# Performance work log

Measured on AMD Instinct MI355X. Metric: run time of the kernel, lower is better.

## Reference

```python
import jax, jax.numpy as jnp
import numpy as np

N_HEAD = 16

def setup_inputs() -> dict:
    key = jax.random.key(0)
    ks = jax.random.split(key, 5)
    B, T, D = 2, 2048, 1024
    k = D // N_HEAD
    scale = 0.02
    return {
        'x': jax.random.normal(ks[0], (B, T, D), dtype=jnp.float32),
        'Wq': jax.random.normal(ks[1], (D, D), dtype=jnp.float32) * scale,
        'Wk': jax.random.normal(ks[2], (D, k), dtype=jnp.float32) * scale,
        'Wv': jax.random.normal(ks[3], (D, k), dtype=jnp.float32) * scale,
        'Wo': jax.random.normal(ks[4], (D, D), dtype=jnp.float32) * scale,
    }

def reference(x, Wq, Wk, Wv, Wo):
    B, T, D = x.shape
    h = N_HEAD
    k = D // h
    Q = (x @ Wq).reshape(B, T, h, k)          # per-head queries
    K = x @ Wk                                 # single shared K head: (B,T,k)
    V = x @ Wv                                 # single shared V head: (B,T,k)
    scores = jnp.einsum('bthk,bsk->bhts', Q, K) / jnp.sqrt(jnp.float32(k))
    causal = jnp.tril(jnp.ones((T, T), dtype=bool))  # (T,T)
    scores = jnp.where(causal[None, None, :, :], scores, -jnp.inf)
    A = jax.nn.softmax(scores, axis=-1)        # (B,h,T,T)
    Y = jnp.einsum('bhts,bsk->bthk', A, V).reshape(B, T, D)
    return Y @ Wo
```

## Files before the change

kernel.cpp:

```cpp
#include <hip/hip_runtime.h>
#include <hip/hip_bf16.h>
#include <stdint.h>

typedef short short8 __attribute__((ext_vector_type(8)));
typedef float f32x4 __attribute__((ext_vector_type(4)));

constexpr int SEQ   = 2048;
constexpr int DM    = 1024;
constexpr int NHEAD = 16;
constexpr int HD    = 64;
constexpr int LDQ   = 1152;
constexpr int BATCH = 2;

__device__ __forceinline__ unsigned short f2bf(float f) {
    union { float f; uint32_t u; } v; v.f = f;
    uint32_t u = v.u;
    uint32_t r = (u + 0x7fffu + ((u >> 16) & 1u)) >> 16;
    return (unsigned short)r;
}

typedef __attribute__((address_space(1))) const void gvoid_t;
typedef __attribute__((address_space(3))) void lvoid_t;
__device__ __forceinline__ void gload16(const void* g, void* l) {
    __builtin_amdgcn_global_load_lds((gvoid_t*)g, (lvoid_t*)l, 16, 0, 0);
}

__global__ __launch_bounds__(256) void cast_x_kernel(
        const float* __restrict__ x, unsigned short* __restrict__ xb, int n) {
    int i = (blockIdx.x * 256 + threadIdx.x) * 4;
    if (i >= n) return;
    const float4 v = *(const float4*)(x + i);
    ushort4 o;
    o.x = f2bf(v.x); o.y = f2bf(v.y); o.z = f2bf(v.z); o.w = f2bf(v.w);
    *(ushort4*)(xb + i) = o;
}

__global__ __launch_bounds__(256) void prep_w_kernel(
        const float* __restrict__ Wq, const float* __restrict__ Wk,
        const float* __restrict__ Wv, const float* __restrict__ Wo,
        unsigned short* __restrict__ wtq, unsigned short* __restrict__ wot) {
    __shared__ unsigned short tile[32][33];
    int z = blockIdx.z;
    const float* W; unsigned short* Wt; int C;
    if (z == 0)      { W = Wq; Wt = wtq;                              C = DM; }
    else if (z == 1) { W = Wk; Wt = wtq + (size_t)DM * DM;            C = HD; }
    else if (z == 2) { W = Wv; Wt = wtq + (size_t)(DM + HD) * DM;     C = HD; }
    else             { W = Wo; Wt = wot;                              C = DM; }
    int c0 = blockIdx.x * 32, r0 = blockIdx.y * 32;
    if (c0 >= C) return;
    int tx = threadIdx.x & 31, ty = threadIdx.x >> 5;
    for (int i = ty; i < 32; i += 8)
        tile[i][tx] = f2bf(W[(size_t)(r0 + i) * C + (c0 + tx)]);
    __syncthreads();
    for (int i = ty; i < 32; i += 8)
        Wt[(size_t)(c0 + i) * DM + (r0 + tx)] = tile[tx][i];
}

__global__ __launch_bounds__(256) void gemm_bt_kernel(
        const unsigned short* __restrict__ A,
        const unsigned short* __restrict__ Bt,
        void* __restrict__ Cout,
        unsigned short* __restrict__ VtOut,
        int M, int N, int K, int out_bf16) {
    __shared__ unsigned short ldsA[2][2][128 * 32];
    __shared__ unsigned short ldsB[2][2][64 * 32];
    int lane = threadIdx.x & 63, wave = threadIdx.x >> 6;
    int ln = lane & 15, quad = lane >> 4;
    int wm = wave >> 1, wn = wave & 1;
    int m0 = blockIdx.y * 128, n0 = blockIdx.x * 64;

    int srow = lane >> 2, scol = (lane & 3) * 8;
    const unsigned short* gA0 = A + (size_t)(m0 + wave * 32 + srow) * K + scol;
    const unsigned short* gA1 = gA0 + (size_t)16 * K;
    const unsigned short* gB0 = Bt + (size_t)(n0 + wave * 16 + srow) * K + scol;

    f32x4 acc[4][2];
    for (int i = 0; i < 4; ++i)
        for (int jj = 0; jj < 2; ++jj) acc[i][jj] = f32x4{0, 0, 0, 0};

    auto stage = [&](int k0, int buf) {
#pragma unroll
        for (int hh = 0; hh < 2; ++hh) {
            gload16(gA0 + k0 + hh * 32, &ldsA[buf][hh][wave * 1024]);
            gload16(gA1 + k0 + hh * 32, &ldsA[buf][hh][wave * 1024 + 512]);
            gload16(gB0 + k0 + hh * 32, &ldsB[buf][hh][wave * 512]);
        }
    };

    stage(0, 0);
    int niter = K >> 6;
    for (int it = 0; it < niter; ++it) {
        __syncthreads();
        if (it + 1 < niter) stage((it + 1) << 6, (it + 1) & 1);
        int buf = it & 1;
        short8 aF[2][4], bF[2][2];
#pragma unroll
        for (int hh = 0; hh < 2; ++hh) {
#pragma unroll
            for (int i = 0; i < 4; ++i)
                aF[hh][i] = *(const short8*)&ldsA[buf][hh][(wm * 64 + i * 16 + ln) * 32 + quad * 8];
#pragma unroll
            for (int jj = 0; jj < 2; ++jj)
                bF[hh][jj] = *(const short8*)&ldsB[buf][hh][(wn * 32 + jj * 16 + ln) * 32 + quad * 8];
        }
#pragma unroll
        for (int hh = 0; hh < 2; ++hh)
#pragma unroll
            for (int mt = 0; mt < 4; ++mt)
#pragma unroll
                for (int nt = 0; nt < 2; ++nt)
                    acc[mt][nt] = __builtin_amdgcn_mfma_f32_16x16x32_bf16(
                        aF[hh][mt], bF[hh][nt], acc[mt][nt], 0, 0, 0);
    }

    if (out_bf16) {
        unsigned short* C = (unsigned short*)Cout;
#pragma unroll
        for (int mt = 0; mt < 4; ++mt)
            for (int nt = 0; nt < 2; ++nt)
                for (int r = 0; r < 4; ++r) {
                    int row = m0 + wm * 64 + mt * 16 + quad * 4 + r;
                    int col = n0 + wn * 32 + nt * 16 + ln;
                    C[(size_t)row * N + col] = f2bf(acc[mt][nt][r]);
                }
        if (VtOut != nullptr && n0 == DM + HD) {
#pragma unroll
            for (int mt = 0; mt < 4; ++mt)
                for (int nt = 0; nt < 2; ++nt)
                    for (int r = 0; r < 4; ++r) {
                        int row = m0 + wm * 64 + mt * 16 + quad * 4 + r;
                        int d = wn * 32 + nt * 16 + ln;
                        int bb = row >> 11, s = row & 2047;
                        VtOut[((size_t)bb * HD + d) * SEQ + s] = f2bf(acc[mt][nt][r]);
                    }
        }
    } else {
        float* C = (float*)Cout;
#pragma unroll
        for (int mt = 0; mt < 4; ++mt)
            for (int nt = 0; nt < 2; ++nt)
                for (int r = 0; r < 4; ++r) {
                    int row = m0 + wm * 64 + mt * 16 + quad * 4 + r;
                    int col = n0 + wn * 32 + nt * 16 + ln;
                    C[(size_t)row * N + col] = acc[mt][nt][r];
                }
    }
}

__global__ __launch_bounds__(256) void attn_kernel(
        const unsigned short* __restrict__ QKV,
        const unsigned short* __restrict__ Vt,
        unsigned short* __restrict__ Y) {
    __shared__ unsigned short ldsK[2][64 * 64];
    __shared__ unsigned short ldsV[2][64 * 64];
    __shared__ unsigned short pbuf[4][16][72];

    int lane = threadIdx.x & 63, wave = threadIdx.x >> 6;
    int ln = lane & 15, quad = lane >> 4;
    int bid = blockIdx.x;
    int jg = 31 - (bid >> 5);
    int bh = bid & 31;
    int h = bh & 15, b = bh >> 4;
    int q0 = (jg * 4 + wave) * 16;
    const size_t baseRow = (size_t)b * SEQ;
    const unsigned short* Vb = Vt + (size_t)b * HD * SEQ;

    int t = threadIdx.x;
    int trow = t >> 3, tcb = t & 7;
    int cbg = tcb ^ (trow & 7);
    const unsigned short* gK = QKV + (baseRow + trow) * LDQ + DM + cbg * 8;
    const unsigned short* gV = Vb + (size_t)trow * SEQ + cbg * 8;
    int dstoff = trow * 64 + tcb * 8;

    auto stageKV = [&](int s0n, int buf) {
#pragma unroll
        for (int rr = 0; rr < 2; ++rr) {
            gload16(gK + (size_t)(s0n + 32 * rr) * LDQ, &ldsK[buf][dstoff + rr * 2048]);
            gload16(gV + (size_t)32 * rr * SEQ + s0n,   &ldsV[buf][dstoff + rr * 2048]);
        }
    };

    short8 aQ0, aQ1;
    {
        const unsigned short* qp = QKV + (baseRow + q0 + ln) * LDQ + h * HD + quad * 8;
        aQ0 = *(const short8*)(qp);
        aQ1 = *(const short8*)(qp + 32);
    }

    float lsum[4] = {0.f, 0.f, 0.f, 0.f};
    f32x4 o[4];
    for (int nt = 0; nt < 4; ++nt) o[nt] = f32x4{0, 0, 0, 0};

    const float c_exp = 0.1803368802f;

    auto computeStep = [&](int s0, int buf, bool partial) {
        const unsigned short* Kb = ldsK[buf];
        const unsigned short* Vf = ldsV[buf];
#pragma unroll
        for (int c = 0; c < 4; ++c) {
            int kbase = s0 + c * 16;
            if (partial && kbase > q0 + 15) {
#pragma unroll
                for (int r = 0; r < 4; ++r)
                    pbuf[wave][quad * 4 + r][c * 16 + ln] = 0;
                continue;
            }
            short8 k0f = *(const short8*)&Kb[(c * 16 + ln) * 64 + ((quad ^ (ln & 7)) * 8)];
            short8 k1f = *(const short8*)&Kb[(c * 16 + ln) * 64 + (((4 + quad) ^ (ln & 7)) * 8)];
            f32x4 s = {0, 0, 0, 0};
            s = __builtin_amdgcn_mfma_f32_16x16x32_bf16(aQ0, k0f, s, 0, 0, 0);
            s = __builtin_amdgcn_mfma_f32_16x16x32_bf16(aQ1, k1f, s, 0, 0, 0);
            bool diag = partial && (kbase + 15 > q0);
#pragma unroll
            for (int r = 0; r < 4; ++r) {
                float e = __builtin_exp2f(s[r] * c_exp);
                if (diag && (kbase + ln > q0 + quad * 4 + r)) e = 0.f;
                lsum[r] += e;
                pbuf[wave][quad * 4 + r][c * 16 + ln] =
                    (unsigned short)(__float_as_uint(e) >> 16);
            }
        }
        short8 aP0 = *(const short8*)&pbuf[wave][ln][quad * 8];
        short8 aP1 = *(const short8*)&pbuf[wave][ln][32 + quad * 8];
#pragma unroll
        for (int nt = 0; nt < 4; ++nt) {
            short8 v0 = *(const short8*)&Vf[(nt * 16 + ln) * 64 + ((quad ^ (ln & 7)) * 8)];
            short8 v1 = *(const short8*)&Vf[(nt * 16 + ln) * 64 + (((4 + quad) ^ (ln & 7)) * 8)];
            o[nt] = __builtin_amdgcn_mfma_f32_16x16x32_bf16(aP0, v0, o[nt], 0, 0, 0);
            o[nt] = __builtin_amdgcn_mfma_f32_16x16x32_bf16(aP1, v1, o[nt], 0, 0, 0);
        }
    };

    stageKV(0, 0);
    for (int it = 0; it < jg; ++it) {
        __syncthreads();
        stageKV((it + 1) * 64, (it + 1) & 1);
        computeStep(it * 64, it & 1, false);
    }
    __syncthreads();
    computeStep(jg * 64, jg & 1, true);

    for (int off = 1; off < 16; off <<= 1)
#pragma unroll
        for (int r = 0; r < 4; ++r) lsum[r] += __shfl_xor(lsum[r], off);
#pragma unroll
    for (int r = 0; r < 4; ++r) {
        float inv = 1.0f / lsum[r];
        int t_idx = q0 + quad * 4 + r;
        unsigned short* yp = Y + (baseRow + t_idx) * DM + h * HD + ln;
        for (int nt = 0; nt < 4; ++nt)
            yp[nt * 16] = f2bf(o[nt][r] * inv);
    }
}

extern "C" void kernel_launch(void* const* d_in, const int* in_sizes, int n_in,
                              void* d_out, int out_size, void* d_ws, size_t ws_size,
                              hipStream_t stream) {
    const float* x  = (const float*)d_in[0];
    const float* Wq = (const float*)d_in[1];
    const float* Wk = (const float*)d_in[2];
    const float* Wv = (const float*)d_in[3];
    const float* Wo = (const float*)d_in[4];
    float* out = (float*)d_out;

    char* ws = (char*)d_ws;
    unsigned short* xb  = (unsigned short*)(ws);
    unsigned short* y   = (unsigned short*)(ws);
    unsigned short* wtq = (unsigned short*)(ws + 8388608);
    unsigned short* wot = (unsigned short*)(ws + 10747904);
    unsigned short* qkv = (unsigned short*)(ws + 12845056);
    unsigned short* Vt  = (unsigned short*)(ws + 22282240);

    const int BT = BATCH * SEQ;

    hipLaunchKernelGGL(cast_x_kernel, dim3(BT * DM / 4 / 256), dim3(256), 0, stream,
                       x, xb, BT * DM);
    hipLaunchKernelGGL(prep_w_kernel, dim3(DM / 32, DM / 32, 4), dim3(256), 0, stream,
                       Wq, Wk, Wv, Wo, wtq, wot);

    hipLaunchKernelGGL(gemm_bt_kernel, dim3(LDQ / 64, BT / 128), dim3(256), 0, stream,
                       xb, wtq, (void*)qkv, Vt, BT, LDQ, DM, 1);

    hipLaunchKernelGGL(attn_kernel, dim3(32 * 32), dim3(256), 0, stream,
                       qkv, Vt, y);

    hipLaunchKernelGGL(gemm_bt_kernel, dim3(DM / 64, BT / 128), dim3(256), 0, stream,
                       y, wot, (void*)out, nullptr, BT, DM, DM, 0);
}
```

Baseline: 173.5 us.

## Shrink GEMM tile to 64x64 with XOR-swizzled LDS and swizzle attention P buffer

The GEMM drops from 128x64 to 64x64 output tiles per block, which doubles the grid so more blocks fill the CUs. LDS staging changes to a single 64-wide K slab per buffer with an XOR swizzle on the column blocks to avoid bank conflicts on fragment reads. The attention kernel's P scratch buffer moves from padded rows to the same XOR-swizzled 64-wide layout. Smaller tiles lower data reuse per block and add global traffic in exchange for more parallelism.

```diff
diff --git a/kernel.cpp b/kernel.cpp
--- a/kernel.cpp
+++ b/kernel.cpp
@@ -62,51 +62,57 @@
         void* __restrict__ Cout,
         unsigned short* __restrict__ VtOut,
         int M, int N, int K, int out_bf16) {
-    __shared__ unsigned short ldsA[2][2][128 * 32];
-    __shared__ unsigned short ldsB[2][2][64 * 32];
+    __shared__ unsigned short ldsA[2][64 * 64];
+    __shared__ unsigned short ldsB[2][64 * 64];
     int lane = threadIdx.x & 63, wave = threadIdx.x >> 6;
     int ln = lane & 15, quad = lane >> 4;
     int wm = wave >> 1, wn = wave & 1;
-    int m0 = blockIdx.y * 128, n0 = blockIdx.x * 64;
-
-    int srow = lane >> 2, scol = (lane & 3) * 8;
-    const unsigned short* gA0 = A + (size_t)(m0 + wave * 32 + srow) * K + scol;
-    const unsigned short* gA1 = gA0 + (size_t)16 * K;
-    const unsigned short* gB0 = Bt + (size_t)(n0 + wave * 16 + srow) * K + scol;
-
-    f32x4 acc[4][2];
-    for (int i = 0; i < 4; ++i)
+    int m0 = blockIdx.y * 64, n0 = blockIdx.x * 64;
+
+    int t = threadIdx.x;
+    int trow = t >> 3, tcb = t & 7;
+    int gcb = tcb ^ (trow & 7);
+    const unsigned short* gA = A + (size_t)(m0 + trow) * K + gcb * 8;
+    const unsigned short* gA2 = gA + (size_t)32 * K;
+    const unsigned short* gB = Bt + (size_t)(n0 + trow) * K + gcb * 8;
+    const unsigned short* gB2 = gB + (size_t)32 * K;
+    int dst = t * 8;
+
+    auto stage = [&](int k0, int buf) {
+        gload16(gA + k0, &ldsA[buf][dst]);
+        gload16(gA2 + k0, &ldsA[buf][dst + 2048]);
+        gload16(gB + k0, &ldsB[buf][dst]);
+        gload16(gB2 + k0, &ldsB[buf][dst + 2048]);
+    };
+
+    f32x4 acc[2][2];
+    for (int i = 0; i < 2; ++i)
         for (int jj = 0; jj < 2; ++jj) acc[i][jj] = f32x4{0, 0, 0, 0};
-
-    auto stage = [&](int k0, int buf) {
-#pragma unroll
-        for (int hh = 0; hh < 2; ++hh) {
-            gload16(gA0 + k0 + hh * 32, &ldsA[buf][hh][wave * 1024]);
-            gload16(gA1 + k0 + hh * 32, &ldsA[buf][hh][wave * 1024 + 512]);
-            gload16(gB0 + k0 + hh * 32, &ldsB[buf][hh][wave * 512]);
-        }
-    };
 
     stage(0, 0);
     int niter = K >> 6;
     for (int it = 0; it < niter; ++it) {
         __syncthreads();
         if (it + 1 < niter) stage((it + 1) << 6, (it + 1) & 1);
-        int buf = it & 1;
-        short8 aF[2][4], bF[2][2];
+        const unsigned short* La = ldsA[it & 1];
+        const unsigned short* Lb = ldsB[it & 1];
+        short8 aF[2][2], bF[2][2];
 #pragma unroll
         for (int hh = 0; hh < 2; ++hh) {
-#pragma unroll
-            for (int i = 0; i < 4; ++i)
-                aF[hh][i] = *(const short8*)&ldsA[buf][hh][(wm * 64 + i * 16 + ln) * 32 + quad * 8];
-#pragma unroll
-            for (int jj = 0; jj < 2; ++jj)
-                bF[hh][jj] = *(const short8*)&ldsB[buf][hh][(wn * 32 + jj * 16 + ln) * 32 + quad * 8];
+            int kc = hh * 4 + quad;
+#pragma unroll
+            for (int mt = 0; mt < 2; ++mt)
+                aF[hh][mt] = *(const short8*)&La[(wm * 32 + mt * 16 + ln) * 64 +
+                                                ((kc ^ (ln & 7)) * 8)];
+#pragma unroll
+            for (int nt = 0; nt < 2; ++nt)
+                bF[hh][nt] = *(const short8*)&Lb[(wn * 32 + nt * 16 + ln) * 64 +
+                                                ((kc ^ (ln & 7)) * 8)];
         }
 #pragma unroll
         for (int hh = 0; hh < 2; ++hh)
 #pragma unroll
-            for (int mt = 0; mt < 4; ++mt)
+            for (int mt = 0; mt < 2; ++mt)
 #pragma unroll
                 for (int nt = 0; nt < 2; ++nt)
                     acc[mt][nt] = __builtin_amdgcn_mfma_f32_16x16x32_bf16(
@@ -116,19 +122,19 @@
     if (out_bf16) {
         unsigned short* C = (unsigned short*)Cout;
 #pragma unroll
-        for (int mt = 0; mt < 4; ++mt)
+        for (int mt = 0; mt < 2; ++mt)
             for (int nt = 0; nt < 2; ++nt)
                 for (int r = 0; r < 4; ++r) {
-                    int row = m0 + wm * 64 + mt * 16 + quad * 4 + r;
+                    int row = m0 + wm * 32 + mt * 16 + quad * 4 + r;
                     int col = n0 + wn * 32 + nt * 16 + ln;
                     C[(size_t)row * N + col] = f2bf(acc[mt][nt][r]);
                 }
         if (VtOut != nullptr && n0 == DM + HD) {
 #pragma unroll
-            for (int mt = 0; mt < 4; ++mt)
+            for (int mt = 0; mt < 2; ++mt)
                 for (int nt = 0; nt < 2; ++nt)
                     for (int r = 0; r < 4; ++r) {
-                        int row = m0 + wm * 64 + mt * 16 + quad * 4 + r;
+                        int row = m0 + wm * 32 + mt * 16 + quad * 4 + r;
                         int d = wn * 32 + nt * 16 + ln;
                         int bb = row >> 11, s = row & 2047;
                         VtOut[((size_t)bb * HD + d) * SEQ + s] = f2bf(acc[mt][nt][r]);
@@ -137,10 +143,10 @@
     } else {
         float* C = (float*)Cout;
 #pragma unroll
-        for (int mt = 0; mt < 4; ++mt)
+        for (int mt = 0; mt < 2; ++mt)
             for (int nt = 0; nt < 2; ++nt)
                 for (int r = 0; r < 4; ++r) {
-                    int row = m0 + wm * 64 + mt * 16 + quad * 4 + r;
+                    int row = m0 + wm * 32 + mt * 16 + quad * 4 + r;
                     int col = n0 + wn * 32 + nt * 16 + ln;
                     C[(size_t)row * N + col] = acc[mt][nt][r];
                 }
@@ -153,7 +159,7 @@
         unsigned short* __restrict__ Y) {
     __shared__ unsigned short ldsK[2][64 * 64];
     __shared__ unsigned short ldsV[2][64 * 64];
-    __shared__ unsigned short pbuf[4][16][72];
+    __shared__ unsigned short pbuf[4][16 * 64];
 
     int lane = threadIdx.x & 63, wave = threadIdx.x >> 6;
     int ln = lane & 15, quad = lane >> 4;
@@ -192,6 +198,7 @@
     for (int nt = 0; nt < 4; ++nt) o[nt] = f32x4{0, 0, 0, 0};
 
     const float c_exp = 0.1803368802f;
+    unsigned short* pb = &pbuf[wave][0];
 
     auto computeStep = [&](int s0, int buf, bool partial) {
         const unsigned short* Kb = ldsK[buf];
@@ -201,8 +208,10 @@
             int kbase = s0 + c * 16;
             if (partial && kbase > q0 + 15) {
 #pragma unroll
-                for (int r = 0; r < 4; ++r)
-                    pbuf[wave][quad * 4 + r][c * 16 + ln] = 0;
+                for (int r = 0; r < 4; ++r) {
+                    int row = quad * 4 + r;
+                    pb[row * 64 + (((c * 2 + (ln >> 3)) ^ (row & 7)) * 8) + (ln & 7)] = 0;
+                }
                 continue;
             }
             short8 k0f = *(const short8*)&Kb[(c * 16 + ln) * 64 + ((quad ^ (ln & 7)) * 8)];
@@ -216,12 +225,13 @@
                 float e = __builtin_exp2f(s[r] * c_exp);
                 if (diag && (kbase + ln > q0 + quad * 4 + r)) e = 0.f;
                 lsum[r] += e;
-                pbuf[wave][quad * 4 + r][c * 16 + ln] =
+                int row = quad * 4 + r;
+                pb[row * 64 + (((c * 2 + (ln >> 3)) ^ (row & 7)) * 8) + (ln & 7)] =
                     (unsigned short)(__float_as_uint(e) >> 16);
             }
         }
-        short8 aP0 = *(const short8*)&pbuf[wave][ln][quad * 8];
-        short8 aP1 = *(const short8*)&pbuf[wave][ln][32 + quad * 8];
+        short8 aP0 = *(const short8*)&pb[ln * 64 + ((quad ^ (ln & 7)) * 8)];
+        short8 aP1 = *(const short8*)&pb[ln * 64 + (((4 + quad) ^ (ln & 7)) * 8)];
 #pragma unroll
         for (int nt = 0; nt < 4; ++nt) {
             short8 v0 = *(const short8*)&Vf[(nt * 16 + ln) * 64 + ((quad ^ (ln & 7)) * 8)];
@@ -278,12 +288,12 @@
     hipLaunchKernelGGL(prep_w_kernel, dim3(DM / 32, DM / 32, 4), dim3(256), 0, stream,
                        Wq, Wk, Wv, Wo, wtq, wot);
 
-    hipLaunchKernelGGL(gemm_bt_kernel, dim3(LDQ / 64, BT / 128), dim3(256), 0, stream,
+    hipLaunchKernelGGL(gemm_bt_kernel, dim3(LDQ / 64, BT / 64), dim3(256), 0, stream,
                        xb, wtq, (void*)qkv, Vt, BT, LDQ, DM, 1);
 
     hipLaunchKernelGGL(attn_kernel, dim3(32 * 32), dim3(256), 0, stream,
                        qkv, Vt, y);
 
-    hipLaunchKernelGGL(gemm_bt_kernel, dim3(DM / 64, BT / 128), dim3(256), 0, stream,
+    hipLaunchKernelGGL(gemm_bt_kernel, dim3(DM / 64, BT / 64), dim3(256), 0, stream,
                        y, wot, (void*)out, nullptr, BT, DM, DM, 0);
 }
```

Measured after the change: 168.4 us. -2.9%, faster.
